# Optimization experiments

Measured on AMD Instinct MI355X. Metric: run time of the kernel, lower is better.

## Reference

```python
import jax, jax.numpy as jnp
import numpy as np

VOLRADIUS = 256.0
DT = 1.0 / VOLRADIUS  # self.dt = dt / volradius with dt=1.0
N_STEPS = 64
B, H, W, K, M = 1, 256, 256, 64, 16


def setup_inputs() -> dict:
    rng = np.random.default_rng(0)
    # orthographic-ish ray bundle looking down +z through the primitive cloud
    ys, xs = np.meshgrid(np.linspace(-1., 1., H, dtype=np.float32),
                         np.linspace(-1., 1., W, dtype=np.float32), indexing='ij')
    raypos = np.broadcast_to(np.stack([xs, ys, np.full_like(xs, -0.125)], -1)[None],
                             (B, H, W, 3)).astype(np.float32).copy()
    raydir = np.zeros((B, H, W, 3), np.float32); raydir[..., 2] = 1.0
    tmin = np.zeros((B, H, W), np.float32)
    tminmax = np.stack([tmin, tmin + N_STEPS * DT], -1).astype(np.float32)
    # primpos is in WORLD units (module divides by volradius)
    primpos = rng.uniform(-0.1 * VOLRADIUS, 0.1 * VOLRADIUS, (B, K, 3)).astype(np.float32)
    q, _ = np.linalg.qr(rng.normal(size=(B, K, 3, 3)))
    primrot = q.astype(np.float32)
    primscale = rng.uniform(8., 16., (B, K, 3)).astype(np.float32)  # inverse half-extent
    primrgba = rng.uniform(0., 1., (B, K, 4, M, M, M)).astype(np.float32)
    return {
        'raypos': jnp.asarray(raypos), 'raydir': jnp.asarray(raydir),
        'tminmax': jnp.asarray(tminmax), 'primpos': jnp.asarray(primpos),
        'primrot': jnp.asarray(primrot), 'primscale': jnproundtrip(primscale) if False else jnp.asarray(primscale),
        'primrgba': jnp.asarray(primrgba),
    }


def _trilinear_sum(template, pos, primpos, primrot, primscale):
    # template [K,4,M,M,M]; pos [R,3]; returns summed rgba over primitives [R,4]
    Mv = template.shape[-1]
    kidx = jnp.arange(template.shape[0])[None, :]                      # [1,K]
    rel = pos[:, None, :] - primpos[None, :, :]                        # [R,K,3]
    # local = primscale * (primrot^T @ rel), inside prim iff |local| < 1
    local = jnp.einsum('kij,rki->rkj', primrot, rel) * primscale[None]  # [R,K,3]
    inside = jnp.all(jnp.abs(local) < 1.0, axis=-1)                    # [R,K]
    g = jnp.clip((local + 1.0) * 0.5 * (Mv - 1), 0.0, Mv - 1 - 1e-5)    # voxel coords (x,y,z)
    i0 = jnp.clip(jnp.floor(g).astype(jnp.int32), 0, Mv - 2)
    f = g - i0.astype(g.dtype)
    x0, y0, z0 = i0[..., 0], i0[..., 1], i0[..., 2]
    fx, fy, fz = f[..., 0], f[..., 1], f[..., 2]
    c = jnp.zeros(local.shape[:2] + (4,), template.dtype)
    for dz, wz in ((0, 1 - fz), (1, fz)):
        for dy, wy in ((0, 1 - fy), (1, fy)):
            for dx, wx in ((0, 1 - fx), (1, fx)):
                corner = template[kidx, :, z0 + dz, y0 + dy, x0 + dx]  # [R,K,4]
                c = c + corner * (wz * wy * wx)[..., None]
    c = c * inside[..., None]
    return c.sum(axis=1)                                               # [R,4]


def _march(raypos, raydir, tminmax, primpos, primrot, primscale, template):
    Hh, Ww, _ = raypos.shape
    R = Hh * Ww
    o = raypos.reshape(R, 3)
    d = raydir.reshape(R, 3)
    tmm = tminmax.reshape(R, 2)
    tmin, tmax = tmm[:, 0], tmm[:, 1]

    def step(carry, i):
        rgb, alpha = carry
        t = tmin + (i.astype(jnp.float32) + 0.5) * DT
        valid = t < tmax
        pos = o + t[:, None] * d
        s = _trilinear_sum(template, pos, primpos, primrot, primscale)  # [R,4]
        # MVP front-to-back saturating alpha compositing (early-term equivalent)
        contrib = jnp.minimum(1.0, alpha + s[:, 3] * DT) - alpha
        contrib = jnp.where(valid, contrib, 0.0)
        rgb = rgb + s[:, :3] * contrib[:, None]
        alpha = alpha + contrib
        return (rgb, alpha), None

    init = (jnp.zeros((R, 3), jnp.float32), jnp.zeros((R,), jnp.float32))
    (rgb, alpha), _ = jax.lax.scan(jax.checkpoint(step), init, jnp.arange(N_STEPS))
    return jnp.concatenate([rgb, alpha[:, None]], -1).reshape(Hh, Ww, 4)


def reference(raypos, raydir, tminmax, primpos, primrot, primscale, primrgba):
    primpos_n = primpos / VOLRADIUS  # module normalizes primpos by volume radius
    rayrgba = jax.vmap(_march)(raypos, raydir, tminmax, primpos_n, primrot, primscale, primrgba)
    rayrgba = jnp.transpose(rayrgba, (0, 3, 1, 2))  # [B,4,H,W]
    rayrgb = rayrgba[:, :3]
    rayalpha = rayrgba[:, 3:4]
    return rayrgb, rayalpha, rayrgba
```

## Files before the change

### kernel.cpp

```cpp
#include <hip/hip_runtime.h>
#include <hip/hip_fp16.h>

#define Rtot 65536
#define Wimg 256
#define Kp 64
#define NSTEPS 64
#define DTc (1.0f/256.0f)
#define INV_VOLR (1.0f/256.0f)
#define NITEMS 16384

#define PD_OFF    0u
#define TB_OFF    4096u
#define FLAG_OFF  20480u
#define TT_OFF    65536u
#define SBUF_OFF  8388608u
#define WS_NEED   (SBUF_OFF + (size_t)NITEMS*256*8)

typedef _Float16 half2v __attribute__((ext_vector_type(2)));

__device__ __forceinline__ half2v u2h(unsigned int u) {
  union { unsigned int u; half2v h; } x; x.u = u; return x.h;
}
__device__ __forceinline__ half2v mkh2(float a, float b) {
  half2v h; h.x = (_Float16)a; h.y = (_Float16)b; return h;
}
__device__ __forceinline__ unsigned int pack2(float a, float b) {
  __half2 h = __floats2half2_rn(a, b);
  return *(unsigned int*)&h;
}

#if __has_builtin(__builtin_amdgcn_fdot2)
#define FDOT2(a, b, c) __builtin_amdgcn_fdot2((a), (b), (c), false)
#else
#define FDOT2(a, b, c) ((float)(a).x*(float)(b).x + (float)(a).y*(float)(b).y + (c))
#endif

__global__ __launch_bounds__(256) void setup_kernel(
    const float* __restrict__ raypos, const float* __restrict__ raydir,
    const float* __restrict__ tminmax, const float* __restrict__ primpos,
    const float* __restrict__ primrot, const float* __restrict__ primscale,
    const float* __restrict__ tmpl,
    float* __restrict__ tb, uint4* __restrict__ tth, float* __restrict__ pd) {
  int bid = blockIdx.x, tid = threadIdx.x;
  if (bid < 256) {
    __shared__ float smn[4][7], smx[4][7];
    int w = (bid & 15)*16 + (tid & 15);
    int h = (bid >> 4)*16 + (tid >> 4);
    int r = h*Wimg + w;
    float v[7];
    v[0] = raypos[r*3+0]; v[1] = raypos[r*3+1]; v[2] = raypos[r*3+2];
    v[3] = raydir[r*3+0]; v[4] = raydir[r*3+1]; v[5] = raydir[r*3+2];
    v[6] = tminmax[r*2+0];
    float mn[7], mx[7];
#pragma unroll
    for (int i = 0; i < 7; ++i) { mn[i] = v[i]; mx[i] = v[i]; }
#pragma unroll
    for (int m = 1; m < 64; m <<= 1) {
#pragma unroll
      for (int i = 0; i < 7; ++i) {
        mn[i] = fminf(mn[i], __shfl_xor(mn[i], m));
        mx[i] = fmaxf(mx[i], __shfl_xor(mx[i], m));
      }
    }
    int wv = tid >> 6;
    if ((tid & 63) == 0) {
#pragma unroll
      for (int i = 0; i < 7; ++i) { smn[wv][i] = mn[i]; smx[wv][i] = mx[i]; }
    }
    __syncthreads();
    if (tid == 0) {
#pragma unroll
      for (int i = 0; i < 7; ++i) {
        tb[bid*16 + i]     = fminf(fminf(smn[0][i], smn[1][i]), fminf(smn[2][i], smn[3][i]));
        tb[bid*16 + 8 + i] = fmaxf(fmaxf(smx[0][i], smx[1][i]), fmaxf(smx[2][i], smx[3][i]));
      }
    }
  } else if (bid < 320) {
    int k = bid - 256;
    const float* b0 = tmpl + (((size_t)k) << 14);
    uint4* o = tth + (k << 12);
    for (int v = tid; v < 4096; v += 256) {
      int x = v & 15;
      int xn = (x < 15) ? v + 1 : v;
      uint4 q;
      q.x = pack2(b0[v],         b0[xn]);
      q.y = pack2(b0[4096+v],    b0[4096+xn]);
      q.z = pack2(b0[8192+v],    b0[8192+xn]);
      q.w = pack2(b0[12288+v],   b0[12288+xn]);
      o[v] = q;
    }
  } else {
    int k = tid;
    if (k < Kp) {
      float sc0 = primscale[k*3+0], sc1 = primscale[k*3+1], sc2 = primscale[k*3+2];
      float* o = pd + (k << 4);
      o[0] = primpos[k*3+0] * INV_VOLR;
      o[1] = primpos[k*3+1] * INV_VOLR;
      o[2] = primpos[k*3+2] * INV_VOLR;
      o[3] = 0.0f; o[4] = 0.0f; o[5] = 0.0f;
#pragma unroll
      for (int i = 0; i < 3; ++i) {
        o[6+i*3+0] = primrot[k*9+i*3+0]*sc0;
        o[6+i*3+1] = primrot[k*9+i*3+1]*sc1;
        o[6+i*3+2] = primrot[k*9+i*3+2]*sc2;
      }
      o[15] = 0.0f;
    }
  }
}

#define PRIM_SETUP(S, K)                                                     \
  { const float* p = pd + ((K) << 4);                                        \
    float relx = px - p[0], rely = py - p[1], relz = pz - p[2];              \
    float lx = relx*p[6] + rely*p[9]  + relz*p[12];                          \
    float ly = relx*p[7] + rely*p[10] + relz*p[13];                          \
    float lz = relx*p[8] + rely*p[11] + relz*p[14];                          \
    bool inside = fabsf(lx) < 1.0f && fabsf(ly) < 1.0f && fabsf(lz) < 1.0f;  \
    any##S = __any(inside);                                                  \
    float gx = fminf(fmaxf((lx + 1.0f)*7.5f, 0.0f), 14.99999f);              \
    float gy = fminf(fmaxf((ly + 1.0f)*7.5f, 0.0f), 14.99999f);              \
    float gz = fminf(fmaxf((lz + 1.0f)*7.5f, 0.0f), 14.99999f);              \
    int ix = (int)gx, iy = (int)gy, iz = (int)gz;                            \
    float fx = gx - (float)ix, fy = gy - (float)iy, fz = gz - (float)iz;     \
    float m = inside ? 1.0f : 0.0f;                                          \
    float wy0 = 1.0f - fy, wz0m = (1.0f - fz)*m, fzm = fz*m;                 \
    float wx0 = 1.0f - fx;                                                   \
    float w00 = wz0m*wy0, w01 = wz0m*fy, w10 = fzm*wy0, w11 = fzm*fy;        \
    w2_0##S = mkh2(w00*wx0, w00*fx);                                         \
    w2_1##S = mkh2(w01*wx0, w01*fx);                                         \
    w2_2##S = mkh2(w10*wx0, w10*fx);                                         \
    w2_3##S = mkh2(w11*wx0, w11*fx);                                         \
    const uint4* a = tth + ((size_t)(K) << 12) + (iz*256 + iy*16 + ix);      \
    if (any##S) { q0##S = a[0]; q1##S = a[16]; q2##S = a[256]; q3##S = a[272]; } }

#define PRIM_ACC(S)                                                          \
  if (any##S) {                                                              \
    c0 = FDOT2(u2h(q0##S.x), w2_0##S, c0);                                   \
    c1 = FDOT2(u2h(q0##S.y), w2_0##S, c1);                                   \
    c2 = FDOT2(u2h(q0##S.z), w2_0##S, c2);                                   \
    c3 = FDOT2(u2h(q0##S.w), w2_0##S, c3);                                   \
    c0 = FDOT2(u2h(q1##S.x), w2_1##S, c0);                                   \
    c1 = FDOT2(u2h(q1##S.y), w2_1##S, c1);                                   \
    c2 = FDOT2(u2h(q1##S.z), w2_1##S, c2);                                   \
    c3 = FDOT2(u2h(q1##S.w), w2_1##S, c3);                                   \
    c0 = FDOT2(u2h(q2##S.x), w2_2##S, c0);                                   \
    c1 = FDOT2(u2h(q2##S.y), w2_2##S, c1);                                   \
    c2 = FDOT2(u2h(q2##S.z), w2_2##S, c2);                                   \
    c3 = FDOT2(u2h(q2##S.w), w2_2##S, c3);                                   \
    c0 = FDOT2(u2h(q3##S.x), w2_3##S, c0);                                   \
    c1 = FDOT2(u2h(q3##S.y), w2_3##S, c1);                                   \
    c2 = FDOT2(u2h(q3##S.z), w2_3##S, c2);                                   \
    c3 = FDOT2(u2h(q3##S.w), w2_3##S, c3);                                   \
  }

__global__ __launch_bounds__(256) void shade_kernel(
    const float* __restrict__ raypos, const float* __restrict__ raydir,
    const float* __restrict__ tminmax, const float* __restrict__ pd,
    const float* __restrict__ tb, const uint4* __restrict__ tth,
    unsigned long long* __restrict__ sbuf, unsigned char* __restrict__ flags) {
  __shared__ int s_list[Kp];
  __shared__ int s_cnt;
  int item = blockIdx.x;
  int tile = item >> 6, step = item & 63;
  int tid = threadIdx.x;
  if (tid < 64) {
    const float* t0 = tb + tile*16;
    float cst = ((float)step + 0.5f)*DTc;
    float tl = t0[6] + cst, th = t0[14] + cst;
    const float* p = pd + (tid << 4);
    float rlo[3], rhi[3];
#pragma unroll
    for (int a = 0; a < 3; ++a) {
      float ol = t0[a], oh = t0[8+a], dl = t0[3+a], dh = t0[11+a];
      float p1 = tl*dl, p2 = tl*dh, p3 = th*dl, p4 = th*dh;
      float lo = ol + fminf(fminf(p1, p2), fminf(p3, p4));
      float hi = oh + fmaxf(fmaxf(p1, p2), fmaxf(p3, p4));
      rlo[a] = lo - p[a];
      rhi[a] = hi - p[a];
    }
    bool pass = true;
#pragma unroll
    for (int j = 0; j < 3; ++j) {
      float llo = 0.f, lhi = 0.f;
#pragma unroll
      for (int a = 0; a < 3; ++a) {
        float rsc = p[6+a*3+j];
        float q1 = rlo[a]*rsc, q2 = rhi[a]*rsc;
        llo += fminf(q1, q2);
        lhi += fmaxf(q1, q2);
      }
      pass = pass && (llo < 1.0f) && (lhi > -1.0f);
    }
    unsigned long long mask = __ballot(pass);
    if (tid == 0) s_cnt = (int)__popcll(mask);
    if (pass) {
      int pos = (int)__popcll(mask & ((1ull << tid) - 1ull));
      s_list[pos] = tid;
    }
  }
  __syncthreads();
  int cnt = s_cnt;
  if (tid == 0) flags[item] = (unsigned char)(cnt > 0 ? 1 : 0);
  if (cnt == 0) return;

  int w = (tile & 15)*16 + (tid & 15);
  int h = (tile >> 4)*16 + (tid >> 4);
  int r = h*Wimg + w;
  float t = __builtin_nontemporal_load(&tminmax[r*2]) + ((float)step + 0.5f)*DTc;
  float px = fmaf(t, __builtin_nontemporal_load(&raydir[r*3+0]),
                     __builtin_nontemporal_load(&raypos[r*3+0]));
  float py = fmaf(t, __builtin_nontemporal_load(&raydir[r*3+1]),
                     __builtin_nontemporal_load(&raypos[r*3+1]));
  float pz = fmaf(t, __builtin_nontemporal_load(&raydir[r*3+2]),
                     __builtin_nontemporal_load(&raypos[r*3+2]));
  float c0 = 0.f, c1 = 0.f, c2 = 0.f, c3 = 0.f;

  bool anyA, anyB;
  uint4 q0A, q1A, q2A, q3A, q0B, q1B, q2B, q3B;
  half2v w2_0A, w2_1A, w2_2A, w2_3A, w2_0B, w2_1B, w2_2B, w2_3B;

  int k = __builtin_amdgcn_readfirstlane(s_list[0]);
  PRIM_SETUP(A, k)
  int j = 1;
  while (j + 1 < cnt) {
    k = __builtin_amdgcn_readfirstlane(s_list[j]);
    PRIM_SETUP(B, k)
    PRIM_ACC(A)
    k = __builtin_amdgcn_readfirstlane(s_list[j+1]);
    PRIM_SETUP(A, k)
    PRIM_ACC(B)
    j += 2;
  }
  if (j < cnt) {
    k = __builtin_amdgcn_readfirstlane(s_list[j]);
    PRIM_SETUP(B, k)
    PRIM_ACC(A)
    PRIM_ACC(B)
  } else {
    PRIM_ACC(A)
  }

  unsigned long long pk = ((unsigned long long)pack2(c2, c3) << 32)
                        | (unsigned long long)pack2(c0, c1);
  __builtin_nontemporal_store(pk, &sbuf[item*256 + tid]);
}

__global__ __launch_bounds__(256) void composite_kernel(
    const float* __restrict__ tminmax, const unsigned long long* __restrict__ sbuf,
    const unsigned char* __restrict__ flags, float* __restrict__ out) {
  __shared__ unsigned char s_flags[NSTEPS];
  int tid = threadIdx.x;
  int b = blockIdx.x;
  if (tid < NSTEPS) s_flags[tid] = flags[b*NSTEPS + tid];
  __syncthreads();
  int w = (b & 15)*16 + (tid & 15);
  int h = (b >> 4)*16 + (tid >> 4);
  int r = h*Wimg + w;
  float tmin = tminmax[r*2+0], tmax = tminmax[r*2+1];
  float rgb0 = 0.f, rgb1 = 0.f, rgb2 = 0.f, alpha = 0.f;
  for (int i = 0; i < NSTEPS; ++i) {
    float s0 = 0.f, s1 = 0.f, s2 = 0.f, s3 = 0.f;
    if (s_flags[i]) {
      unsigned long long pk = __builtin_nontemporal_load(&sbuf[(b*NSTEPS + i)*256 + tid]);
      unsigned int lo = (unsigned int)pk, hi = (unsigned int)(pk >> 32);
      float2 lf = __half22float2(*(__half2*)&lo);
      float2 hf = __half22float2(*(__half2*)&hi);
      s0 = lf.x; s1 = lf.y; s2 = hf.x; s3 = hf.y;
    }
    float t = tmin + ((float)i + 0.5f)*DTc;
    float contrib = fminf(1.0f, fmaf(s3, DTc, alpha)) - alpha;
    contrib = (t < tmax) ? contrib : 0.0f;
    rgb0 = fmaf(s0, contrib, rgb0);
    rgb1 = fmaf(s1, contrib, rgb1);
    rgb2 = fmaf(s2, contrib, rgb2);
    alpha += contrib;
  }
  __builtin_nontemporal_store(rgb0,  &out[0*Rtot + r]);
  __builtin_nontemporal_store(rgb1,  &out[1*Rtot + r]);
  __builtin_nontemporal_store(rgb2,  &out[2*Rtot + r]);
  __builtin_nontemporal_store(alpha, &out[3*Rtot + r]);
  __builtin_nontemporal_store(rgb0,  &out[4*Rtot + r]);
  __builtin_nontemporal_store(rgb1,  &out[5*Rtot + r]);
  __builtin_nontemporal_store(rgb2,  &out[6*Rtot + r]);
  __builtin_nontemporal_store(alpha, &out[7*Rtot + r]);
}

__global__ __launch_bounds__(256) void fallback_kernel(
    const float* __restrict__ raypos, const float* __restrict__ raydir,
    const float* __restrict__ tminmax,
    const float* __restrict__ primpos, const float* __restrict__ primrot,
    const float* __restrict__ primscale, const float* __restrict__ tmpl,
    float* __restrict__ out) {
  __shared__ float s_pd[Kp][16];
  int tx = threadIdx.x, ty = threadIdx.y;
  int tid = ty*16 + tx;
  if (tid < Kp) {
    int k = tid;
    float sc0 = primscale[k*3+0], sc1 = primscale[k*3+1], sc2 = primscale[k*3+2];
    s_pd[k][0] = primpos[k*3+0]*INV_VOLR;
    s_pd[k][1] = primpos[k*3+1]*INV_VOLR;
    s_pd[k][2] = primpos[k*3+2]*INV_VOLR;
#pragma unroll
    for (int i = 0; i < 3; ++i) {
      s_pd[k][6+i*3+0] = primrot[k*9+i*3+0]*sc0;
      s_pd[k][6+i*3+1] = primrot[k*9+i*3+1]*sc1;
      s_pd[k][6+i*3+2] = primrot[k*9+i*3+2]*sc2;
    }
  }
  __syncthreads();
  int w = blockIdx.x*16 + tx, h = blockIdx.y*16 + ty;
  int r = h*Wimg + w;
  float ox = raypos[r*3+0], oy = raypos[r*3+1], oz = raypos[r*3+2];
  float dx = raydir[r*3+0], dy = raydir[r*3+1], dz = raydir[r*3+2];
  float tmin = tminmax[r*2+0], tmax = tminmax[r*2+1];
  float rgb0=0.f, rgb1=0.f, rgb2=0.f, alpha=0.f;
  for (int i = 0; i < NSTEPS; ++i) {
    float t = tmin + ((float)i + 0.5f)*DTc;
    float px = fmaf(t, dx, ox), py = fmaf(t, dy, oy), pz = fmaf(t, dz, oz);
    float c[4] = {0.f, 0.f, 0.f, 0.f};
    for (int k = 0; k < Kp; ++k) {
      const float* p = &s_pd[k][0];
      float relx = px - p[0], rely = py - p[1], relz = pz - p[2];
      float lx = relx*p[6] + rely*p[9]  + relz*p[12];
      float ly = relx*p[7] + rely*p[10] + relz*p[13];
      float lz = relx*p[8] + rely*p[11] + relz*p[14];
      if (!(fabsf(lx) < 1.0f && fabsf(ly) < 1.0f && fabsf(lz) < 1.0f)) continue;
      float gx = fminf(fmaxf((lx + 1.0f)*7.5f, 0.0f), 14.99999f);
      float gy = fminf(fmaxf((ly + 1.0f)*7.5f, 0.0f), 14.99999f);
      float gz = fminf(fmaxf((lz + 1.0f)*7.5f, 0.0f), 14.99999f);
      int ix = (int)gx, iy = (int)gy, iz = (int)gz;
      ix = ix > 14 ? 14 : ix; iy = iy > 14 ? 14 : iy; iz = iz > 14 ? 14 : iz;
      float fx = gx - (float)ix, fy = gy - (float)iy, fz = gz - (float)iz;
      float wx0 = 1.0f - fx, wy0 = 1.0f - fy, wz0 = 1.0f - fz;
      float w00 = wz0*wy0, w01 = wz0*fy, w10 = fz*wy0, w11 = fz*fy;
      const float* base = tmpl + (((size_t)k) << 14) + iz*256 + iy*16 + ix;
#pragma unroll
      for (int ch = 0; ch < 4; ++ch) {
        const float* bb = base + ch*4096;
        c[ch] += (bb[0]  *wx0 + bb[1]  *fx) * w00
               + (bb[16] *wx0 + bb[17] *fx) * w01
               + (bb[256]*wx0 + bb[257]*fx) * w10
               + (bb[272]*wx0 + bb[273]*fx) * w11;
      }
    }
    float contrib = fminf(1.0f, fmaf(c[3], DTc, alpha)) - alpha;
    contrib = (t < tmax) ? contrib : 0.0f;
    rgb0 = fmaf(c[0], contrib, rgb0);
    rgb1 = fmaf(c[1], contrib, rgb1);
    rgb2 = fmaf(c[2], contrib, rgb2);
    alpha += contrib;
  }
  out[0*Rtot + r] = rgb0;
  out[1*Rtot + r] = rgb1;
  out[2*Rtot + r] = rgb2;
  out[3*Rtot + r] = alpha;
  out[4*Rtot + r] = rgb0;
  out[5*Rtot + r] = rgb1;
  out[6*Rtot + r] = rgb2;
  out[7*Rtot + r] = alpha;
}

extern "C" void kernel_launch(void* const* d_in, const int* in_sizes, int n_in,
                              void* d_out, int out_size, void* d_ws, size_t ws_size,
                              hipStream_t stream) {
  const float* raypos    = (const float*)d_in[0];
  const float* raydir    = (const float*)d_in[1];
  const float* tminmax   = (const float*)d_in[2];
  const float* primpos   = (const float*)d_in[3];
  const float* primrot   = (const float*)d_in[4];
  const float* primscale = (const float*)d_in[5];
  const float* primrgba  = (const float*)d_in[6];
  float* out = (float*)d_out;

  if (ws_size >= WS_NEED) {
    char* ws = (char*)d_ws;
    float* pd            = (float*)(ws + PD_OFF);
    float* tb            = (float*)(ws + TB_OFF);
    unsigned char* flags = (unsigned char*)(ws + FLAG_OFF);
    uint4* tth           = (uint4*)(ws + TT_OFF);
    unsigned long long* sbuf = (unsigned long long*)(ws + SBUF_OFF);

    setup_kernel<<<321, 256, 0, stream>>>(raypos, raydir, tminmax, primpos,
                                          primrot, primscale, primrgba,
                                          tb, tth, pd);
    shade_kernel<<<NITEMS, 256, 0, stream>>>(raypos, raydir, tminmax, pd, tb,
                                             tth, sbuf, flags);
    composite_kernel<<<256, 256, 0, stream>>>(tminmax, sbuf, flags, out);
  } else {
    fallback_kernel<<<dim3(16,16), dim3(16,16), 0, stream>>>(
        raypos, raydir, tminmax, primpos, primrot, primscale, primrgba, out);
  }
}
```

Before: 84.02 us.

## Cull primitives per wavefront with exact sample bounds and triple-buffer prim pipeline

The shade kernel now builds a separate primitive list for each 64-lane wavefront. Each list is culled against the exact bounding box of that wavefront's sample positions, found with shuffle reductions, instead of one conservative list per block from the tile's ray-bundle bounds. The per-primitive __any branch is removed; padded and out-of-count primitives are masked by a zero weight, and the software pipeline goes from 2 to 3 stages with loads issued unconditionally. Nontemporal loads and stores are replaced with ordinary ones. Fewer primitives per wave should cut texture fetches, at the cost of an extra reduction, a per-wave ballot, and unconditional loads even when no lane is inside a primitive.

```diff
diff --git a/kernel.cpp b/kernel.cpp
--- a/kernel.cpp
+++ b/kernel.cpp
@@ -109,20 +109,19 @@
   }
 }
 
-#define PRIM_SETUP(S, K)                                                     \
-  { const float* p = pd + ((K) << 4);                                        \
+#define PRIM_SETUP(S, kk, vm)                                                \
+  { const float* p = pd + ((kk) << 4);                                       \
     float relx = px - p[0], rely = py - p[1], relz = pz - p[2];              \
     float lx = relx*p[6] + rely*p[9]  + relz*p[12];                          \
     float ly = relx*p[7] + rely*p[10] + relz*p[13];                          \
     float lz = relx*p[8] + rely*p[11] + relz*p[14];                          \
     bool inside = fabsf(lx) < 1.0f && fabsf(ly) < 1.0f && fabsf(lz) < 1.0f;  \
-    any##S = __any(inside);                                                  \
     float gx = fminf(fmaxf((lx + 1.0f)*7.5f, 0.0f), 14.99999f);              \
     float gy = fminf(fmaxf((ly + 1.0f)*7.5f, 0.0f), 14.99999f);              \
     float gz = fminf(fmaxf((lz + 1.0f)*7.5f, 0.0f), 14.99999f);              \
     int ix = (int)gx, iy = (int)gy, iz = (int)gz;                            \
     float fx = gx - (float)ix, fy = gy - (float)iy, fz = gz - (float)iz;     \
-    float m = inside ? 1.0f : 0.0f;                                          \
+    float m = inside ? (vm) : 0.0f;                                          \
     float wy0 = 1.0f - fy, wz0m = (1.0f - fz)*m, fzm = fz*m;                 \
     float wx0 = 1.0f - fx;                                                   \
     float w00 = wz0m*wy0, w01 = wz0m*fy, w10 = fzm*wy0, w11 = fzm*fy;        \
@@ -130,12 +129,11 @@
     w2_1##S = mkh2(w01*wx0, w01*fx);                                         \
     w2_2##S = mkh2(w10*wx0, w10*fx);                                         \
     w2_3##S = mkh2(w11*wx0, w11*fx);                                         \
-    const uint4* a = tth + ((size_t)(K) << 12) + (iz*256 + iy*16 + ix);      \
-    if (any##S) { q0##S = a[0]; q1##S = a[16]; q2##S = a[256]; q3##S = a[272]; } }
+    const uint4* a = tth + ((size_t)(kk) << 12) + (iz*256 + iy*16 + ix);     \
+    q0##S = a[0]; q1##S = a[16]; q2##S = a[256]; q3##S = a[272]; }
 
 #define PRIM_ACC(S)                                                          \
-  if (any##S) {                                                              \
-    c0 = FDOT2(u2h(q0##S.x), w2_0##S, c0);                                   \
+  { c0 = FDOT2(u2h(q0##S.x), w2_0##S, c0);                                   \
     c1 = FDOT2(u2h(q0##S.y), w2_0##S, c1);                                   \
     c2 = FDOT2(u2h(q0##S.z), w2_0##S, c2);                                   \
     c3 = FDOT2(u2h(q0##S.w), w2_0##S, c3);                                   \
@@ -150,19 +148,20 @@
     c0 = FDOT2(u2h(q3##S.x), w2_3##S, c0);                                   \
     c1 = FDOT2(u2h(q3##S.y), w2_3##S, c1);                                   \
     c2 = FDOT2(u2h(q3##S.z), w2_3##S, c2);                                   \
-    c3 = FDOT2(u2h(q3##S.w), w2_3##S, c3);                                   \
-  }
+    c3 = FDOT2(u2h(q3##S.w), w2_3##S, c3); }
 
 __global__ __launch_bounds__(256) void shade_kernel(
     const float* __restrict__ raypos, const float* __restrict__ raydir,
     const float* __restrict__ tminmax, const float* __restrict__ pd,
     const float* __restrict__ tb, const uint4* __restrict__ tth,
     unsigned long long* __restrict__ sbuf, unsigned char* __restrict__ flags) {
-  __shared__ int s_list[Kp];
-  __shared__ int s_cnt;
+  __shared__ int s_any;
+  __shared__ int s_list[4][66];
   int item = blockIdx.x;
   int tile = item >> 6, step = item & 63;
   int tid = threadIdx.x;
+  int lane = tid & 63, wv = tid >> 6;
+
   if (tid < 64) {
     const float* t0 = tb + tile*16;
     float cst = ((float)step + 0.5f)*DTc;
@@ -173,10 +172,8 @@
     for (int a = 0; a < 3; ++a) {
       float ol = t0[a], oh = t0[8+a], dl = t0[3+a], dh = t0[11+a];
       float p1 = tl*dl, p2 = tl*dh, p3 = th*dl, p4 = th*dh;
-      float lo = ol + fminf(fminf(p1, p2), fminf(p3, p4));
-      float hi = oh + fmaxf(fmaxf(p1, p2), fmaxf(p3, p4));
-      rlo[a] = lo - p[a];
-      rhi[a] = hi - p[a];
+      rlo[a] = ol + fminf(fminf(p1, p2), fminf(p3, p4)) - p[a];
+      rhi[a] = oh + fmaxf(fmaxf(p1, p2), fmaxf(p3, p4)) - p[a];
     }
     bool pass = true;
 #pragma unroll
@@ -192,57 +189,91 @@
       pass = pass && (llo < 1.0f) && (lhi > -1.0f);
     }
     unsigned long long mask = __ballot(pass);
-    if (tid == 0) s_cnt = (int)__popcll(mask);
-    if (pass) {
-      int pos = (int)__popcll(mask & ((1ull << tid) - 1ull));
-      s_list[pos] = tid;
-    }
+    if (tid == 0) s_any = (mask != 0ull);
   }
   __syncthreads();
-  int cnt = s_cnt;
-  if (tid == 0) flags[item] = (unsigned char)(cnt > 0 ? 1 : 0);
-  if (cnt == 0) return;
+  if (!s_any) {
+    if (tid == 0) flags[item] = 0;
+    return;
+  }
+  if (tid == 0) flags[item] = 1;
 
   int w = (tile & 15)*16 + (tid & 15);
   int h = (tile >> 4)*16 + (tid >> 4);
   int r = h*Wimg + w;
-  float t = __builtin_nontemporal_load(&tminmax[r*2]) + ((float)step + 0.5f)*DTc;
-  float px = fmaf(t, __builtin_nontemporal_load(&raydir[r*3+0]),
-                     __builtin_nontemporal_load(&raypos[r*3+0]));
-  float py = fmaf(t, __builtin_nontemporal_load(&raydir[r*3+1]),
-                     __builtin_nontemporal_load(&raypos[r*3+1]));
-  float pz = fmaf(t, __builtin_nontemporal_load(&raydir[r*3+2]),
-                     __builtin_nontemporal_load(&raypos[r*3+2]));
-  float c0 = 0.f, c1 = 0.f, c2 = 0.f, c3 = 0.f;
-
-  bool anyA, anyB;
-  uint4 q0A, q1A, q2A, q3A, q0B, q1B, q2B, q3B;
-  half2v w2_0A, w2_1A, w2_2A, w2_3A, w2_0B, w2_1B, w2_2B, w2_3B;
-
-  int k = __builtin_amdgcn_readfirstlane(s_list[0]);
-  PRIM_SETUP(A, k)
-  int j = 1;
-  while (j + 1 < cnt) {
-    k = __builtin_amdgcn_readfirstlane(s_list[j]);
-    PRIM_SETUP(B, k)
-    PRIM_ACC(A)
-    k = __builtin_amdgcn_readfirstlane(s_list[j+1]);
-    PRIM_SETUP(A, k)
-    PRIM_ACC(B)
-    j += 2;
-  }
-  if (j < cnt) {
-    k = __builtin_amdgcn_readfirstlane(s_list[j]);
-    PRIM_SETUP(B, k)
-    PRIM_ACC(A)
-    PRIM_ACC(B)
-  } else {
-    PRIM_ACC(A)
-  }
-
-  unsigned long long pk = ((unsigned long long)pack2(c2, c3) << 32)
-                        | (unsigned long long)pack2(c0, c1);
-  __builtin_nontemporal_store(pk, &sbuf[item*256 + tid]);
+  float t = tminmax[r*2] + ((float)step + 0.5f)*DTc;
+  float px = fmaf(t, raydir[r*3+0], raypos[r*3+0]);
+  float py = fmaf(t, raydir[r*3+1], raypos[r*3+1]);
+  float pz = fmaf(t, raydir[r*3+2], raypos[r*3+2]);
+
+  float bmnx = px, bmny = py, bmnz = pz, bmxx = px, bmxy = py, bmxz = pz;
+#pragma unroll
+  for (int m = 1; m < 64; m <<= 1) {
+    bmnx = fminf(bmnx, __shfl_xor(bmnx, m));
+    bmny = fminf(bmny, __shfl_xor(bmny, m));
+    bmnz = fminf(bmnz, __shfl_xor(bmnz, m));
+    bmxx = fmaxf(bmxx, __shfl_xor(bmxx, m));
+    bmxy = fmaxf(bmxy, __shfl_xor(bmxy, m));
+    bmxz = fmaxf(bmxz, __shfl_xor(bmxz, m));
+  }
+  {
+    const float* p = pd + (lane << 4);
+    float rlo0 = bmnx - p[0], rhi0 = bmxx - p[0];
+    float rlo1 = bmny - p[1], rhi1 = bmxy - p[1];
+    float rlo2 = bmnz - p[2], rhi2 = bmxz - p[2];
+    bool pass = true;
+#pragma unroll
+    for (int j = 0; j < 3; ++j) {
+      float a0 = p[6+j], a1 = p[9+j], a2 = p[12+j];
+      float q1 = rlo0*a0, q2 = rhi0*a0;
+      float llo = fminf(q1, q2), lhi = fmaxf(q1, q2);
+      q1 = rlo1*a1; q2 = rhi1*a1;
+      llo += fminf(q1, q2); lhi += fmaxf(q1, q2);
+      q1 = rlo2*a2; q2 = rhi2*a2;
+      llo += fminf(q1, q2); lhi += fmaxf(q1, q2);
+      pass = pass && (llo < 1.0f) && (lhi > -1.0f);
+    }
+    unsigned long long mask = __ballot(pass);
+    int cnt = (int)__popcll(mask);
+    if (pass) {
+      int pos = (int)__popcll(mask & ((1ull << lane) - 1ull));
+      s_list[wv][pos] = lane;
+    }
+    int cntp = ((cnt + 2) / 3) * 3;
+    if (lane < cntp - cnt) s_list[wv][cnt + lane] = 0;
+
+    float c0 = 0.f, c1 = 0.f, c2 = 0.f, c3 = 0.f;
+    if (cnt > 0) {
+      bool anyA, anyB, anyC; (void)anyA; (void)anyB; (void)anyC;
+      uint4 q0A, q1A, q2A, q3A, q0B, q1B, q2B, q3B, q0C, q1C, q2C, q3C;
+      half2v w2_0A, w2_1A, w2_2A, w2_3A;
+      half2v w2_0B, w2_1B, w2_2B, w2_3B;
+      half2v w2_0C, w2_1C, w2_2C, w2_3C;
+      int kk = __builtin_amdgcn_readfirstlane(s_list[wv][0]);
+      PRIM_SETUP(A, kk, 1.0f)
+      kk = __builtin_amdgcn_readfirstlane(s_list[wv][1]);
+      PRIM_SETUP(B, kk, (1 < cnt) ? 1.0f : 0.0f)
+      kk = __builtin_amdgcn_readfirstlane(s_list[wv][2]);
+      PRIM_SETUP(C, kk, (2 < cnt) ? 1.0f : 0.0f)
+      for (int i = 3; i + 2 < cntp; i += 3) {
+        PRIM_ACC(A)
+        kk = __builtin_amdgcn_readfirstlane(s_list[wv][i]);
+        PRIM_SETUP(A, kk, (i < cnt) ? 1.0f : 0.0f)
+        PRIM_ACC(B)
+        kk = __builtin_amdgcn_readfirstlane(s_list[wv][i+1]);
+        PRIM_SETUP(B, kk, (i+1 < cnt) ? 1.0f : 0.0f)
+        PRIM_ACC(C)
+        kk = __builtin_amdgcn_readfirstlane(s_list[wv][i+2]);
+        PRIM_SETUP(C, kk, (i+2 < cnt) ? 1.0f : 0.0f)
+      }
+      PRIM_ACC(A)
+      PRIM_ACC(B)
+      PRIM_ACC(C)
+    }
+    unsigned long long pk = ((unsigned long long)pack2(c2, c3) << 32)
+                          | (unsigned long long)pack2(c0, c1);
+    sbuf[item*256 + tid] = pk;
+  }
 }
 
 __global__ __launch_bounds__(256) void composite_kernel(
@@ -261,7 +292,7 @@
   for (int i = 0; i < NSTEPS; ++i) {
     float s0 = 0.f, s1 = 0.f, s2 = 0.f, s3 = 0.f;
     if (s_flags[i]) {
-      unsigned long long pk = __builtin_nontemporal_load(&sbuf[(b*NSTEPS + i)*256 + tid]);
+      unsigned long long pk = sbuf[(b*NSTEPS + i)*256 + tid];
       unsigned int lo = (unsigned int)pk, hi = (unsigned int)(pk >> 32);
       float2 lf = __half22float2(*(__half2*)&lo);
       float2 hf = __half22float2(*(__half2*)&hi);
@@ -275,14 +306,14 @@
     rgb2 = fmaf(s2, contrib, rgb2);
     alpha += contrib;
   }
-  __builtin_nontemporal_store(rgb0,  &out[0*Rtot + r]);
-  __builtin_nontemporal_store(rgb1,  &out[1*Rtot + r]);
-  __builtin_nontemporal_store(rgb2,  &out[2*Rtot + r]);
-  __builtin_nontemporal_store(alpha, &out[3*Rtot + r]);
-  __builtin_nontemporal_store(rgb0,  &out[4*Rtot + r]);
-  __builtin_nontemporal_store(rgb1,  &out[5*Rtot + r]);
-  __builtin_nontemporal_store(rgb2,  &out[6*Rtot + r]);
-  __builtin_nontemporal_store(alpha, &out[7*Rtot + r]);
+  out[0*Rtot + r] = rgb0;
+  out[1*Rtot + r] = rgb1;
+  out[2*Rtot + r] = rgb2;
+  out[3*Rtot + r] = alpha;
+  out[4*Rtot + r] = rgb0;
+  out[5*Rtot + r] = rgb1;
+  out[6*Rtot + r] = rgb2;
+  out[7*Rtot + r] = alpha;
 }
 
 __global__ __launch_bounds__(256) void fallback_kernel(
```

After: 73.43 us. 12.6% less time.
